# Kernel tuning notes

Measured on AMD Instinct MI355X. Metric: run time of the kernel, lower is better.

## Reference

```python
import jax, jax.numpy as jnp
import numpy as np

NEG_INF = -1e9


def setup_inputs() -> dict:
    key0 = jax.random.key(0)
    ks = jax.random.split(key0, 7)
    B, Tq, Tv, D, U = 8, 512, 512, 512, 128
    query = jax.random.normal(ks[0], (B, Tq, D), dtype=jnp.float32)
    key = jax.random.normal(ks[1], (B, Tv, D), dtype=jnp.float32)
    value = jax.random.normal(ks[2], (B, Tv, D), dtype=jnp.float32)
    mask = jax.random.randint(ks[3], (B, Tv), 0, 2).astype(bool)
    mask = mask.at[:, 0].set(True)  # ensure no fully-masked row
    Wa = jax.random.normal(ks[4], (D, U), dtype=jnp.float32) * (1.0 / np.sqrt(D))
    Ua = jax.random.normal(ks[5], (D, U), dtype=jnp.float32) * (1.0 / np.sqrt(D))
    scale = jax.random.normal(ks[6], (U,), dtype=jnp.float32) * 0.1
    return {"query": query, "key": key, "value": value, "mask": mask,
            "Wa": Wa, "Ua": Ua, "scale": scale}


def reference(query, key, value, mask, Wa, Ua, scale):
    # Dense projections (no bias)
    q = query @ Wa          # [B, Tq, U]
    k = key @ Ua            # [B, Tv, U]
    # Additive (Bahdanau) scores with learned per-unit scale:
    # scores[b,i,j] = sum_u scale[u] * tanh(q[b,i,u] + k[b,j,u])
    t = jnp.tanh(q[:, :, None, :] + k[:, None, :, :])   # [B, Tq, Tv, U]
    scores = jnp.einsum('bijU,U->bij', t, scale)         # [B, Tq, Tv]
    # Mask padded keys/values then softmax over Tv
    scores = jnp.where(mask[:, None, :], scores, NEG_INF)
    weights = jax.nn.softmax(scores, axis=-1)            # [B, Tq, Tv]
    # Weighted sum of values (query_mask is all-True in source -> no-op)
    context = jnp.einsum('bij,bjd->bid', weights, value) # [B, Tq, D]
    return context
```

## Files before the change

### kernel.cpp

```cpp
#include <hip/hip_runtime.h>

constexpr int Bb = 8;
constexpr int Tq = 512;
constexpr int Tv = 512;
constexpr int Dd = 512;
constexpr int Uu = 128;
constexpr float C2LOG2E = 2.88539008177792681f;
constexpr float LOG2E   = 1.44269504088896341f;

__global__ __launch_bounds__(256) void proj_kernel(
    const float* __restrict__ query,
    const float* __restrict__ key,
    const float* __restrict__ Wa,
    const float* __restrict__ Ua,
    const int* __restrict__ mask,
    float* __restrict__ qf2, float* __restrict__ kT)
{
    const int R    = blockIdx.x * 16;
    const bool isQ = R < Bb * Tq;
    const float* __restrict__ src = isQ ? query : key;
    const float* __restrict__ W   = isQ ? Wa : Ua;
    const int Rloc = isQ ? R : R - Bb * Tq;

    __shared__ float x[16 * Dd];
    __shared__ int posLoc[16];
    const int t = threadIdx.x;

    {
        const float4* __restrict__ s4 =
            reinterpret_cast<const float4*>(src + (size_t)Rloc * Dd);
        float4* x4 = reinterpret_cast<float4*>(x);
#pragma unroll
        for (int m = 0; m < 8; ++m) x4[t + 256 * m] = s4[t + 256 * m];
    }
    if (!isQ && t < 64) {
        const int b  = Rloc >> 9;
        const int j0 = Rloc & 511;
        int base = 0;
#pragma unroll
        for (int c = 0; c < 8; ++c) {
            const int j = c * 64 + t;
            const int v = (mask[b * 512 + j] != 0);
            const unsigned long long bits = __ballot(v);
            const int pos = base + (int)__popcll(bits & ((1ull << t) - 1ull));
            if (j >= j0 && j < j0 + 16) posLoc[j - j0] = v ? pos : -1;
            base += (int)__popcll(bits);
        }
    }
    __syncthreads();

    const int ub = t & 63;
    const int rh = t >> 6;
    float acc[4][2] = {{0,0},{0,0},{0,0},{0,0}};

#pragma unroll 2
    for (int d4 = 0; d4 < Dd / 4; ++d4) {
        const int d = d4 * 4;
        const float w0x = W[(d + 0) * Uu + ub],      w1x = W[(d + 0) * Uu + ub + 64];
        const float w0y = W[(d + 1) * Uu + ub],      w1y = W[(d + 1) * Uu + ub + 64];
        const float w0z = W[(d + 2) * Uu + ub],      w1z = W[(d + 2) * Uu + ub + 64];
        const float w0w = W[(d + 3) * Uu + ub],      w1w = W[(d + 3) * Uu + ub + 64];
#pragma unroll
        for (int k = 0; k < 4; ++k) {
            const float4 xv = *reinterpret_cast<const float4*>(x + (rh * 4 + k) * Dd + d);
            acc[k][0] = fmaf(xv.x, w0x, acc[k][0]);
            acc[k][0] = fmaf(xv.y, w0y, acc[k][0]);
            acc[k][0] = fmaf(xv.z, w0z, acc[k][0]);
            acc[k][0] = fmaf(xv.w, w0w, acc[k][0]);
            acc[k][1] = fmaf(xv.x, w1x, acc[k][1]);
            acc[k][1] = fmaf(xv.y, w1y, acc[k][1]);
            acc[k][1] = fmaf(xv.z, w1z, acc[k][1]);
            acc[k][1] = fmaf(xv.w, w1w, acc[k][1]);
        }
    }

    if (isQ) {
#pragma unroll
        for (int k = 0; k < 4; ++k) {
            const size_t row = (size_t)(Rloc + rh * 4 + k);
            qf2[row * Uu + ub]      = C2LOG2E * acc[k][0];
            qf2[row * Uu + ub + 64] = C2LOG2E * acc[k][1];
        }
    } else {
        float* __restrict__ kb = kT + (size_t)(Rloc >> 9) * Uu * Tv;
        const int u4a = ub >> 2, ca = ub & 3;
#pragma unroll
        for (int k = 0; k < 4; ++k) {
            const int p = posLoc[rh * 4 + k];
            if (p >= 0) {
                kb[(size_t)(u4a        * Tv + p) * 4 + ca] = C2LOG2E * acc[k][0];
                kb[(size_t)((u4a + 16) * Tv + p) * 4 + ca] = C2LOG2E * acc[k][1];
            }
        }
    }
}

__global__ __launch_bounds__(512) void attn_kernel(
    const float* __restrict__ qf2, const float* __restrict__ kT,
    const float* __restrict__ value,
    const int* __restrict__ mask,
    const float* __restrict__ scale,
    float* __restrict__ out)
{
    const int r0 = blockIdx.x * 8;
    const int b  = r0 >> 9;
    const int t  = threadIdx.x;

    __shared__ float q2[8 * Uu];
    __shared__ float s2[Uu];
    __shared__ int   jl[Tv];
    __shared__ float w[8 * Tv];
    __shared__ float pbuf[8 * Dd];
    __shared__ float inv8[8];
    __shared__ int   cntS;

    jl[t] = 0;
    if (t < 256)
        reinterpret_cast<float4*>(q2)[t] =
            reinterpret_cast<const float4*>(qf2 + (size_t)r0 * Uu)[t];
    else if (t < 384) s2[t - 256] = scale[t - 256];
    __syncthreads();
    if (t < 64) {
        int base = 0;
#pragma unroll
        for (int c = 0; c < 8; ++c) {
            const int j = c * 64 + t;
            const int v = (mask[b * 512 + j] != 0);
            const unsigned long long bits = __ballot(v);
            const int pos = base + (int)__popcll(bits & ((1ull << t) - 1ull));
            if (v) jl[pos] = j;
            base += (int)__popcll(bits);
        }
        if (t == 0) cntS = base;
    }
    __syncthreads();

    const int cnt   = cntS;
    const int cntp4 = (cnt + 3) & ~3;

    const int jc = t;
    if (jc < cnt) {
        const float4* __restrict__ kb4 =
            reinterpret_cast<const float4*>(kT) + (size_t)b * 32 * Tv + jc;
        float acc[8] = {0,0,0,0,0,0,0,0};
#pragma unroll 2
        for (int u4 = 0; u4 < Uu / 4; ++u4) {
            const float4 kv = kb4[(size_t)u4 * Tv];
            const float4 sv = reinterpret_cast<const float4*>(s2)[u4];
#pragma unroll
            for (int i = 0; i < 8; ++i) {
                const float4 qv = *reinterpret_cast<const float4*>(q2 + i * Uu + u4 * 4);
                float e0 = __builtin_amdgcn_exp2f(qv.x + kv.x);
                float e1 = __builtin_amdgcn_exp2f(qv.y + kv.y);
                float e2 = __builtin_amdgcn_exp2f(qv.z + kv.z);
                float e3 = __builtin_amdgcn_exp2f(qv.w + kv.w);
                acc[i] = fmaf(sv.x, __builtin_amdgcn_rcpf(e0 + 1.f), acc[i]);
                acc[i] = fmaf(sv.y, __builtin_amdgcn_rcpf(e1 + 1.f), acc[i]);
                acc[i] = fmaf(sv.z, __builtin_amdgcn_rcpf(e2 + 1.f), acc[i]);
                acc[i] = fmaf(sv.w, __builtin_amdgcn_rcpf(e3 + 1.f), acc[i]);
            }
        }
#pragma unroll
        for (int i = 0; i < 8; ++i) w[i * Tv + jc] = -2.f * acc[i];
    } else {
#pragma unroll
        for (int i = 0; i < 8; ++i) w[i * Tv + jc] = 0.f;
    }
    __syncthreads();

    {
        const int wv = t >> 6, ln = t & 63;
        float* __restrict__ row = w + wv * Tv;
        float vals[8];
        float m = -3e38f;
#pragma unroll
        for (int c = 0; c < 8; ++c) {
            const int e = ln + 64 * c;
            vals[c] = (e < cnt) ? row[e] : -3e38f;
            m = fmaxf(m, vals[c]);
        }
#pragma unroll
        for (int off = 32; off; off >>= 1) m = fmaxf(m, __shfl_xor(m, off, 64));
        float sum = 0.f;
#pragma unroll
        for (int c = 0; c < 8; ++c) {
            const int e = ln + 64 * c;
            if (e < cnt) {
                float ex = __builtin_amdgcn_exp2f((vals[c] - m) * LOG2E);
                row[e] = ex;
                sum += ex;
            }
        }
#pragma unroll
        for (int off = 32; off; off >>= 1) sum += __shfl_xor(sum, off, 64);
        if (ln == 0) inv8[wv] = 1.0f / sum;
    }
    __syncthreads();

    const int mid = ((cntp4 >> 1) + 3) & ~3;
    const int g  = t >> 8;
    const int c  = t & 255;
    const int d0 = c * 2;
    const int jbeg = g ? mid : 0;
    const int jend = g ? cntp4 : mid;
    const float* __restrict__ vb = value + (size_t)b * Tv * Dd + d0;
    float ax[8], ay[8];
#pragma unroll
    for (int i = 0; i < 8; ++i) { ax[i] = 0.f; ay[i] = 0.f; }

    for (int jj = jbeg; jj < jend; jj += 4) {
        const int4 rows = *reinterpret_cast<const int4*>(jl + jj);
        const float2 v0 = *reinterpret_cast<const float2*>(vb + (size_t)rows.x * Dd);
        const float2 v1 = *reinterpret_cast<const float2*>(vb + (size_t)rows.y * Dd);
        const float2 v2 = *reinterpret_cast<const float2*>(vb + (size_t)rows.z * Dd);
        const float2 v3 = *reinterpret_cast<const float2*>(vb + (size_t)rows.w * Dd);
#pragma unroll
        for (int i = 0; i < 8; ++i) {
            const float4 wq = *reinterpret_cast<const float4*>(w + i * Tv + jj);
            ax[i] = fmaf(wq.x, v0.x, ax[i]); ay[i] = fmaf(wq.x, v0.y, ay[i]);
            ax[i] = fmaf(wq.y, v1.x, ax[i]); ay[i] = fmaf(wq.y, v1.y, ay[i]);
            ax[i] = fmaf(wq.z, v2.x, ax[i]); ay[i] = fmaf(wq.z, v2.y, ay[i]);
            ax[i] = fmaf(wq.w, v3.x, ax[i]); ay[i] = fmaf(wq.w, v3.y, ay[i]);
        }
    }

    if (g == 1) {
#pragma unroll
        for (int i = 0; i < 8; ++i) {
            float2 p; p.x = ax[i]; p.y = ay[i];
            *reinterpret_cast<float2*>(pbuf + i * Dd + d0) = p;
        }
    }
    __syncthreads();
    if (g == 0) {
#pragma unroll
        for (int i = 0; i < 8; ++i) {
            const float inv = inv8[i];
            const float2 p1 = *reinterpret_cast<const float2*>(pbuf + i * Dd + d0);
            float2 o;
            o.x = (ax[i] + p1.x) * inv;
            o.y = (ay[i] + p1.y) * inv;
            *reinterpret_cast<float2*>(out + (size_t)(r0 + i) * Dd + d0) = o;
        }
    }
}

extern "C" void kernel_launch(void* const* d_in, const int* in_sizes, int n_in,
                              void* d_out, int out_size, void* d_ws, size_t ws_size,
                              hipStream_t stream)
{
    const float* query = (const float*)d_in[0];
    const float* key   = (const float*)d_in[1];
    const float* value = (const float*)d_in[2];
    const int*   mask  = (const int*)d_in[3];
    const float* Wa    = (const float*)d_in[4];
    const float* Ua    = (const float*)d_in[5];
    const float* scale = (const float*)d_in[6];
    float* out = (float*)d_out;

    float* qf2 = (float*)d_ws;
    float* kT  = qf2 + Bb * Tq * Uu;

    proj_kernel<<<(2 * Bb * Tq) / 16, 256, 0, stream>>>(query, key, Wa, Ua, mask, qf2, kT);
    attn_kernel<<<(Bb * Tq) / 8, 512, 0, stream>>>(qf2, kT, value, mask, scale, out);
}
```

Baseline: 165.6 us.

## Split unit dimension across thread halves in scores and split-K projection

In the attention kernel, the tanh-score stage previously gave one thread per compacted key, which left threads idle for masked keys. It now splits the 128 units into two halves, handled by the two 256-thread groups. The groups loop over compacted keys, write partial sums to two buffers, and those are added during the softmax. The projection kernel now splits the D reduction into four quarters per thread group, with 16 rows per thread, followed by a shared-memory reduction and vectorised float4 stores. This adds extra barriers and shared-memory traffic in exchange for better thread utilisation and fewer redundant weight loads.

```diff
diff --git a/kernel.cpp b/kernel.cpp
--- a/kernel.cpp
+++ b/kernel.cpp
@@ -50,46 +50,73 @@
     __syncthreads();
 
     const int ub = t & 63;
-    const int rh = t >> 6;
-    float acc[4][2] = {{0,0},{0,0},{0,0},{0,0}};
+    const int dq = t >> 6;
+    const float* __restrict__ Wq = W + (size_t)dq * 128 * Uu;
+    const float* __restrict__ xq = x + dq * 128;
+
+    float acc[16][2];
+#pragma unroll
+    for (int r = 0; r < 16; ++r) { acc[r][0] = 0.f; acc[r][1] = 0.f; }
 
 #pragma unroll 2
-    for (int d4 = 0; d4 < Dd / 4; ++d4) {
+    for (int d4 = 0; d4 < 32; ++d4) {
         const int d = d4 * 4;
-        const float w0x = W[(d + 0) * Uu + ub],      w1x = W[(d + 0) * Uu + ub + 64];
-        const float w0y = W[(d + 1) * Uu + ub],      w1y = W[(d + 1) * Uu + ub + 64];
-        const float w0z = W[(d + 2) * Uu + ub],      w1z = W[(d + 2) * Uu + ub + 64];
-        const float w0w = W[(d + 3) * Uu + ub],      w1w = W[(d + 3) * Uu + ub + 64];
-#pragma unroll
-        for (int k = 0; k < 4; ++k) {
-            const float4 xv = *reinterpret_cast<const float4*>(x + (rh * 4 + k) * Dd + d);
-            acc[k][0] = fmaf(xv.x, w0x, acc[k][0]);
-            acc[k][0] = fmaf(xv.y, w0y, acc[k][0]);
-            acc[k][0] = fmaf(xv.z, w0z, acc[k][0]);
-            acc[k][0] = fmaf(xv.w, w0w, acc[k][0]);
-            acc[k][1] = fmaf(xv.x, w1x, acc[k][1]);
-            acc[k][1] = fmaf(xv.y, w1y, acc[k][1]);
-            acc[k][1] = fmaf(xv.z, w1z, acc[k][1]);
-            acc[k][1] = fmaf(xv.w, w1w, acc[k][1]);
-        }
-    }
-
-    if (isQ) {
-#pragma unroll
-        for (int k = 0; k < 4; ++k) {
-            const size_t row = (size_t)(Rloc + rh * 4 + k);
-            qf2[row * Uu + ub]      = C2LOG2E * acc[k][0];
-            qf2[row * Uu + ub + 64] = C2LOG2E * acc[k][1];
-        }
-    } else {
-        float* __restrict__ kb = kT + (size_t)(Rloc >> 9) * Uu * Tv;
-        const int u4a = ub >> 2, ca = ub & 3;
-#pragma unroll
-        for (int k = 0; k < 4; ++k) {
-            const int p = posLoc[rh * 4 + k];
+        const float w0x = Wq[(d + 0) * Uu + ub], w1x = Wq[(d + 0) * Uu + ub + 64];
+        const float w0y = Wq[(d + 1) * Uu + ub], w1y = Wq[(d + 1) * Uu + ub + 64];
+        const float w0z = Wq[(d + 2) * Uu + ub], w1z = Wq[(d + 2) * Uu + ub + 64];
+        const float w0w = Wq[(d + 3) * Uu + ub], w1w = Wq[(d + 3) * Uu + ub + 64];
+#pragma unroll
+        for (int r = 0; r < 16; ++r) {
+            const float4 xv = *reinterpret_cast<const float4*>(xq + r * Dd + d);
+            acc[r][0] = fmaf(xv.x, w0x, acc[r][0]);
+            acc[r][0] = fmaf(xv.y, w0y, acc[r][0]);
+            acc[r][0] = fmaf(xv.z, w0z, acc[r][0]);
+            acc[r][0] = fmaf(xv.w, w0w, acc[r][0]);
+            acc[r][1] = fmaf(xv.x, w1x, acc[r][1]);
+            acc[r][1] = fmaf(xv.y, w1y, acc[r][1]);
+            acc[r][1] = fmaf(xv.z, w1z, acc[r][1]);
+            acc[r][1] = fmaf(xv.w, w1w, acc[r][1]);
+        }
+    }
+
+    __syncthreads();
+    {
+        float* __restrict__ part = x;
+#pragma unroll
+        for (int r = 0; r < 16; ++r) {
+            part[(dq * 16 + r) * 128 + ub]      = acc[r][0];
+            part[(dq * 16 + r) * 128 + ub + 64] = acc[r][1];
+        }
+    }
+    __syncthreads();
+
+    {
+        const float* __restrict__ part = x;
+        const int r  = t >> 4;
+        const int u0 = (t & 15) * 8;
+        float v[8];
+#pragma unroll
+        for (int q = 0; q < 8; ++q) {
+            const float s = part[(0 * 16 + r) * 128 + u0 + q]
+                          + part[(1 * 16 + r) * 128 + u0 + q]
+                          + part[(2 * 16 + r) * 128 + u0 + q]
+                          + part[(3 * 16 + r) * 128 + u0 + q];
+            v[q] = C2LOG2E * s;
+        }
+        if (isQ) {
+            float4* __restrict__ dst =
+                reinterpret_cast<float4*>(qf2 + (size_t)(Rloc + r) * Uu + u0);
+            dst[0] = make_float4(v[0], v[1], v[2], v[3]);
+            dst[1] = make_float4(v[4], v[5], v[6], v[7]);
+        } else {
+            const int p = posLoc[r];
             if (p >= 0) {
-                kb[(size_t)(u4a        * Tv + p) * 4 + ca] = C2LOG2E * acc[k][0];
-                kb[(size_t)((u4a + 16) * Tv + p) * 4 + ca] = C2LOG2E * acc[k][1];
+                float* __restrict__ kb = kT + (size_t)(Rloc >> 9) * Uu * Tv;
+                const int u4a = u0 >> 2;
+                *reinterpret_cast<float4*>(kb + ((size_t)u4a       * Tv + p) * 4) =
+                    make_float4(v[0], v[1], v[2], v[3]);
+                *reinterpret_cast<float4*>(kb + ((size_t)(u4a + 1) * Tv + p) * 4) =
+                    make_float4(v[4], v[5], v[6], v[7]);
             }
         }
     }
@@ -138,45 +165,51 @@
     const int cnt   = cntS;
     const int cntp4 = (cnt + 3) & ~3;
 
-    const int jc = t;
-    if (jc < cnt) {
+    {
+        const int g   = t >> 8;
+        const int jc0 = t & 255;
         const float4* __restrict__ kb4 =
-            reinterpret_cast<const float4*>(kT) + (size_t)b * 32 * Tv + jc;
-        float acc[8] = {0,0,0,0,0,0,0,0};
+            reinterpret_cast<const float4*>(kT) + (size_t)b * 32 * Tv + (size_t)g * 16 * Tv;
+        float* __restrict__ wr = g ? pbuf : w;
+        for (int jb = 0; jb < cnt; jb += 256) {
+            const int jc = jb + jc0;
+            if (jc < cnt) {
+                float acc[8] = {0,0,0,0,0,0,0,0};
 #pragma unroll 2
-        for (int u4 = 0; u4 < Uu / 4; ++u4) {
-            const float4 kv = kb4[(size_t)u4 * Tv];
-            const float4 sv = reinterpret_cast<const float4*>(s2)[u4];
-#pragma unroll
-            for (int i = 0; i < 8; ++i) {
-                const float4 qv = *reinterpret_cast<const float4*>(q2 + i * Uu + u4 * 4);
-                float e0 = __builtin_amdgcn_exp2f(qv.x + kv.x);
-                float e1 = __builtin_amdgcn_exp2f(qv.y + kv.y);
-                float e2 = __builtin_amdgcn_exp2f(qv.z + kv.z);
-                float e3 = __builtin_amdgcn_exp2f(qv.w + kv.w);
-                acc[i] = fmaf(sv.x, __builtin_amdgcn_rcpf(e0 + 1.f), acc[i]);
-                acc[i] = fmaf(sv.y, __builtin_amdgcn_rcpf(e1 + 1.f), acc[i]);
-                acc[i] = fmaf(sv.z, __builtin_amdgcn_rcpf(e2 + 1.f), acc[i]);
-                acc[i] = fmaf(sv.w, __builtin_amdgcn_rcpf(e3 + 1.f), acc[i]);
+                for (int u4 = 0; u4 < 16; ++u4) {
+                    const float4 kv = kb4[(size_t)u4 * Tv + jc];
+                    const float4 sv = reinterpret_cast<const float4*>(s2)[g * 16 + u4];
+#pragma unroll
+                    for (int i = 0; i < 8; ++i) {
+                        const float4 qv = *reinterpret_cast<const float4*>(
+                            q2 + i * Uu + (g * 16 + u4) * 4);
+                        float e0 = __builtin_amdgcn_exp2f(qv.x + kv.x);
+                        float e1 = __builtin_amdgcn_exp2f(qv.y + kv.y);
+                        float e2 = __builtin_amdgcn_exp2f(qv.z + kv.z);
+                        float e3 = __builtin_amdgcn_exp2f(qv.w + kv.w);
+                        acc[i] = fmaf(sv.x, __builtin_amdgcn_rcpf(e0 + 1.f), acc[i]);
+                        acc[i] = fmaf(sv.y, __builtin_amdgcn_rcpf(e1 + 1.f), acc[i]);
+                        acc[i] = fmaf(sv.z, __builtin_amdgcn_rcpf(e2 + 1.f), acc[i]);
+                        acc[i] = fmaf(sv.w, __builtin_amdgcn_rcpf(e3 + 1.f), acc[i]);
+                    }
+                }
+#pragma unroll
+                for (int i = 0; i < 8; ++i) wr[i * Tv + jc] = acc[i];
             }
         }
-#pragma unroll
-        for (int i = 0; i < 8; ++i) w[i * Tv + jc] = -2.f * acc[i];
-    } else {
-#pragma unroll
-        for (int i = 0; i < 8; ++i) w[i * Tv + jc] = 0.f;
     }
     __syncthreads();
 
     {
         const int wv = t >> 6, ln = t & 63;
-        float* __restrict__ row = w + wv * Tv;
+        float* __restrict__ row        = w    + wv * Tv;
+        const float* __restrict__ rowB = pbuf + wv * Tv;
         float vals[8];
         float m = -3e38f;
 #pragma unroll
         for (int c = 0; c < 8; ++c) {
             const int e = ln + 64 * c;
-            vals[c] = (e < cnt) ? row[e] : -3e38f;
+            vals[c] = (e < cnt) ? -2.f * (row[e] + rowB[e]) : -3e38f;
             m = fmaxf(m, vals[c]);
         }
 #pragma unroll
@@ -189,6 +222,8 @@
                 float ex = __builtin_amdgcn_exp2f((vals[c] - m) * LOG2E);
                 row[e] = ex;
                 sum += ex;
+            } else {
+                row[e] = 0.f;
             }
         }
 #pragma unroll
```

New measurement: 172.5 us. 1.04x slower.
